# Kernel optimization log

Measured on AMD Instinct MI355X. Metric: run time of the kernel, lower is better.

The kernel has to match this reference:

```python
import jax, jax.numpy as jnp
import numpy as np

UP_RATIO = 2
DOWN_RATIO = 2
K = 12  # hard-coded filter size assumed by the fused kernel


def kaiser_sinc_filter1d(cutoff, half_width, kernel_size):
    # Exact replica of BigVGAN's kaiser_sinc_filter1d (even kernel branch).
    half_size = kernel_size // 2
    delta_f = 4.0 * half_width
    A = 2.285 * (half_size - 1) * np.pi * delta_f + 7.95
    if A > 50.0:
        beta = 0.1102 * (A - 8.7)
    elif A >= 21.0:
        beta = 0.5842 * (A - 21.0) ** 0.4 + 0.07886 * (A - 21.0)
    else:
        beta = 0.0
    window = np.kaiser(kernel_size, beta)  # symmetric, == torch.kaiser_window(periodic=False)
    time = np.arange(-half_size, half_size) + 0.5  # even kernel size
    filt = 2.0 * cutoff * window * np.sinc(2.0 * cutoff * time)
    filt = filt / filt.sum()
    return filt.astype(np.float32)


def setup_inputs() -> dict:
    key = jax.random.key(0)
    k1, k2, k3 = jax.random.split(key, 3)
    B, C, T = 16, 512, 8192
    x = jax.random.normal(k1, (B, C, T), dtype=jnp.float32)
    # log-scale SnakeBeta parameters (alpha_logscale=True -> params stored in log space)
    alpha = jax.random.normal(k2, (C,), dtype=jnp.float32) * 0.1
    beta = jax.random.normal(k3, (C,), dtype=jnp.float32) * 0.1
    up_filter = jnp.asarray(kaiser_sinc_filter1d(0.5 / UP_RATIO, 0.6 / UP_RATIO, K))
    down_filter = jnp.asarray(kaiser_sinc_filter1d(0.5 / DOWN_RATIO, 0.6 / DOWN_RATIO, K))
    return {"x": x, "up_filter": up_filter, "down_filter": down_filter,
            "alpha": alpha, "beta": beta}


def _depthwise_conv(x, filt, stride=1, lhs_dilation=1, pad=(0, 0)):
    # x: (B, C, T); shared 1-tap-bank depthwise conv: fold channels into batch.
    B, C, T = x.shape
    xr = x.reshape(B * C, 1, T)
    w = filt.reshape(1, 1, -1)
    out = jax.lax.conv_general_dilated(
        xr, w, window_strides=(stride,), padding=[pad],
        lhs_dilation=(lhs_dilation,),
        dimension_numbers=("NCH", "OIH", "NCH"))
    return out.reshape(B, C, -1)


def reference(x, up_filter, down_filter, alpha, beta):
    B, C, T = x.shape
    # ---- UpSample1d(ratio=2, kernel_size=12): replicate pad + conv_transpose ----
    pad = K // UP_RATIO - 1                              # 5
    pad_left = pad * UP_RATIO + (K - UP_RATIO) // 2      # 15
    pad_right = pad * UP_RATIO + (K - UP_RATIO + 1) // 2  # 15
    xp = jnp.pad(x, ((0, 0), (0, 0), (pad, pad)), mode="edge")
    # conv_transpose1d(stride=s) == lhs-dilated conv with flipped kernel, full padding
    up = UP_RATIO * _depthwise_conv(xp, up_filter[::-1],
                                    lhs_dilation=UP_RATIO, pad=(K - 1, K - 1))
    up = up[..., pad_left: up.shape[-1] - pad_right]      # (B, C, 2T)
    # ---- SnakeBeta activation (log-scale alpha/beta) ----
    a = jnp.exp(alpha)[None, :, None]
    b = jnp.exp(beta)[None, :, None]
    act = up + (1.0 / (b + 1e-9)) * jnp.sin(up * a) ** 2
    # ---- DownSample1d: replicate-padded lowpass FIR, stride 2 ----
    dl = K // 2 - 1   # 5 (even kernel)
    dr = K // 2       # 6
    actp = jnp.pad(act, ((0, 0), (0, 0), (dl, dr)), mode="edge")
    out = _depthwise_conv(actp, down_filter, stride=DOWN_RATIO)  # (B, C, T)
    return out
```

## Files before the change

### kernel.cpp

```cpp
#include <hip/hip_runtime.h>


#define T_LEN 8192
#define C_CH  512
#define B_N   16
#define W     8
#define BLOCK 256

__global__ __launch_bounds__(BLOCK) void act1d_kernel(
    const float* __restrict__ x,
    const float* __restrict__ uf_g,
    const float* __restrict__ df_g,
    const float* __restrict__ alpha,
    const float* __restrict__ beta,
    float* __restrict__ out)
{
    const int T = T_LEN;
    const int bid = blockIdx.x;
    const int row = bid >> 2;
    const int chunk = bid & 3;
    const int c = row & (C_CH - 1);
    const int nb = chunk * (BLOCK * W) + (int)threadIdx.x * W;
    const long rowoff = (long)row * T;
    const float* xrow = x + rowoff;

    float uf[12], df[12];
#pragma unroll
    for (int k = 0; k < 12; ++k) { uf[k] = 2.0f * uf_g[k]; df[k] = df_g[k]; }

    const float ea   = __expf(alpha[c]);
    const float invb = 1.0f / (__expf(beta[c]) + 1e-9f);

    float a[26];

    const bool interior = (nb >= 8) && (nb + 16 <= T);
    if (interior) {
        float xr[24];
        const float4* xv = (const float4*)(xrow + nb - 8);
#pragma unroll
        for (int k = 0; k < 6; ++k) {
            float4 v = xv[k];
            xr[4*k+0] = v.x; xr[4*k+1] = v.y; xr[4*k+2] = v.z; xr[4*k+3] = v.w;
        }
#pragma unroll
        for (int j = 0; j < 26; ++j) {
            const int xi = ((j - 5) >> 1) + 8;
            float up;
            if ((j & 1) == 0) {
                up = uf[0]*xr[xi+3] + uf[2]*xr[xi+2] + uf[4]*xr[xi+1]
                   + uf[6]*xr[xi]   + uf[8]*xr[xi-1] + uf[10]*xr[xi-2];
            } else {
                up = uf[1]*xr[xi+2] + uf[3]*xr[xi+1] + uf[5]*xr[xi]
                   + uf[7]*xr[xi-1] + uf[9]*xr[xi-2] + uf[11]*xr[xi-3];
            }
            const float sv = __sinf(up * ea);
            a[j] = fmaf(invb * sv, sv, up);
        }
    } else {
#pragma unroll
        for (int j = 0; j < 26; ++j) {
            int t = 2*nb - 5 + j;
            t = min(max(t, 0), 2*T - 1);
            const int s = t >> 1;
            const int par = t & 1;
            float xv7[7];
#pragma unroll
            for (int m = 0; m < 7; ++m) {
                int g = s - 3 + m;
                g = min(max(g, 0), T - 1);
                xv7[m] = xrow[g];
            }
            const float upo = uf[0]*xv7[6] + uf[2]*xv7[5] + uf[4]*xv7[4]
                            + uf[6]*xv7[3] + uf[8]*xv7[2] + uf[10]*xv7[1];
            const float upe = uf[1]*xv7[5] + uf[3]*xv7[4] + uf[5]*xv7[3]
                            + uf[7]*xv7[2] + uf[9]*xv7[1] + uf[11]*xv7[0];
            const float up = par ? upo : upe;
            const float sv = __sinf(up * ea);
            a[j] = fmaf(invb * sv, sv, up);
        }
    }

    float o[W];
#pragma unroll
    for (int d = 0; d < W; ++d) {
        float acc = 0.0f;
#pragma unroll
        for (int k = 0; k < 12; ++k) acc = fmaf(df[k], a[2*d + k], acc);
        o[d] = acc;
    }
    float4* ov = (float4*)(out + rowoff + nb);
    ov[0] = make_float4(o[0], o[1], o[2], o[3]);
    ov[1] = make_float4(o[4], o[5], o[6], o[7]);
}

extern "C" void kernel_launch(void* const* d_in, const int* in_sizes, int n_in,
                              void* d_out, int out_size, void* d_ws, size_t ws_size,
                              hipStream_t stream) {
    const float* x  = (const float*)d_in[0];
    const float* uf = (const float*)d_in[1];
    const float* df = (const float*)d_in[2];
    const float* al = (const float*)d_in[3];
    const float* be = (const float*)d_in[4];
    float* outp = (float*)d_out;

    const int grid = B_N * C_CH * (T_LEN / (BLOCK * W));
    act1d_kernel<<<grid, BLOCK, 0, stream>>>(x, uf, df, al, be, outp);
}
```

Before: 466.0 us.

## Use packed FP32 math, raw hardware sine, and nontemporal stores in fused kernel

```diff
diff --git a/kernel.cpp b/kernel.cpp
--- a/kernel.cpp
+++ b/kernel.cpp
@@ -6,6 +6,31 @@
 #define B_N   16
 #define W     8
 #define BLOCK 256
+
+typedef float f2 __attribute__((ext_vector_type(2)));
+typedef float f4 __attribute__((ext_vector_type(4)));
+
+__device__ __forceinline__ f2 pk_mul(f2 a, f2 b) {
+    f2 d; asm("v_pk_mul_f32 %0, %1, %2" : "=v"(d) : "v"(a), "v"(b)); return d;
+}
+__device__ __forceinline__ f2 pk_mul_bx(f2 a, f2 b) {
+    f2 d; asm("v_pk_mul_f32 %0, %1, %2 op_sel:[0,0] op_sel_hi:[1,0]" : "=v"(d) : "v"(a), "v"(b)); return d;
+}
+__device__ __forceinline__ f2 pk_mul_by(f2 a, f2 b) {
+    f2 d; asm("v_pk_mul_f32 %0, %1, %2 op_sel:[0,1] op_sel_hi:[1,1]" : "=v"(d) : "v"(a), "v"(b)); return d;
+}
+__device__ __forceinline__ void pk_fma(f2& acc, f2 a, f2 b) {
+    asm("v_pk_fma_f32 %0, %1, %2, %0" : "+v"(acc) : "v"(a), "v"(b));
+}
+__device__ __forceinline__ void pk_fma_bx(f2& acc, f2 a, f2 b) {
+    asm("v_pk_fma_f32 %0, %1, %2, %0 op_sel:[0,0,0] op_sel_hi:[1,0,1]" : "+v"(acc) : "v"(a), "v"(b));
+}
+__device__ __forceinline__ void pk_fma_by(f2& acc, f2 a, f2 b) {
+    asm("v_pk_fma_f32 %0, %1, %2, %0 op_sel:[0,1,0] op_sel_hi:[1,1,1]" : "+v"(acc) : "v"(a), "v"(b));
+}
+__device__ __forceinline__ float hw_sin(float x_rev) {
+    float r; asm("v_sin_f32 %0, %1" : "=v"(r) : "v"(x_rev)); return r;
+}
 
 __global__ __launch_bounds__(BLOCK) void act1d_kernel(
     const float* __restrict__ x,
@@ -24,37 +49,53 @@
     const long rowoff = (long)row * T;
     const float* xrow = x + rowoff;
 
-    float uf[12], df[12];
+    f2 ufp[6], dfp[6];
+    const f2* ufv = (const f2*)uf_g;
+    const f2* dfv = (const f2*)df_g;
 #pragma unroll
-    for (int k = 0; k < 12; ++k) { uf[k] = 2.0f * uf_g[k]; df[k] = df_g[k]; }
+    for (int m = 0; m < 6; ++m) {
+        f2 u = ufv[m];
+        ufp[m].x = 2.0f * u.x; ufp[m].y = 2.0f * u.y;
+        dfp[m] = dfv[m];
+    }
 
-    const float ea   = __expf(alpha[c]);
+    const float ea_r = __expf(alpha[c]) * 0.15915494309189535f;
     const float invb = 1.0f / (__expf(beta[c]) + 1e-9f);
+    f2 eap; eap.x = ea_r; eap.y = ea_r;
+    f2 ibp; ibp.x = invb; ibp.y = invb;
 
-    float a[26];
+    f2 a2[13];
 
     const bool interior = (nb >= 8) && (nb + 16 <= T);
     if (interior) {
-        float xr[24];
-        const float4* xv = (const float4*)(xrow + nb - 8);
+        f2 xx[12];
+        const f4* xv4 = (const f4*)(xrow + nb - 8);
 #pragma unroll
         for (int k = 0; k < 6; ++k) {
-            float4 v = xv[k];
-            xr[4*k+0] = v.x; xr[4*k+1] = v.y; xr[4*k+2] = v.z; xr[4*k+3] = v.w;
+            f4 v = xv4[k];
+            xx[2*k].x   = v.x; xx[2*k].y   = v.y;
+            xx[2*k+1].x = v.z; xx[2*k+1].y = v.w;
         }
 #pragma unroll
-        for (int j = 0; j < 26; ++j) {
-            const int xi = ((j - 5) >> 1) + 8;
-            float up;
-            if ((j & 1) == 0) {
-                up = uf[0]*xr[xi+3] + uf[2]*xr[xi+2] + uf[4]*xr[xi+1]
-                   + uf[6]*xr[xi]   + uf[8]*xr[xi-1] + uf[10]*xr[xi-2];
-            } else {
-                up = uf[1]*xr[xi+2] + uf[3]*xr[xi+1] + uf[5]*xr[xi]
-                   + uf[7]*xr[xi-1] + uf[9]*xr[xi-2] + uf[11]*xr[xi-3];
+        for (int p = 0; p < 13; ++p) {
+            f2 u;
+            {
+                const int w = p + 8;
+                if (w & 1) u = pk_mul_by(ufp[0], xx[w >> 1]);
+                else       u = pk_mul_bx(ufp[0], xx[w >> 1]);
             }
-            const float sv = __sinf(up * ea);
-            a[j] = fmaf(invb * sv, sv, up);
+#pragma unroll
+            for (int m = 1; m < 6; ++m) {
+                const int w = p + 8 - m;
+                if (w & 1) pk_fma_by(u, ufp[m], xx[w >> 1]);
+                else       pk_fma_bx(u, ufp[m], xx[w >> 1]);
+            }
+            f2 s = pk_mul(u, eap);
+            f2 sv; sv.x = hw_sin(s.x); sv.y = hw_sin(s.y);
+            f2 t = pk_mul(sv, ibp);
+            f2 av = u;
+            pk_fma(av, t, sv);
+            a2[p] = av;
         }
     } else {
 #pragma unroll
@@ -70,27 +111,30 @@
                 g = min(max(g, 0), T - 1);
                 xv7[m] = xrow[g];
             }
-            const float upo = uf[0]*xv7[6] + uf[2]*xv7[5] + uf[4]*xv7[4]
-                            + uf[6]*xv7[3] + uf[8]*xv7[2] + uf[10]*xv7[1];
-            const float upe = uf[1]*xv7[5] + uf[3]*xv7[4] + uf[5]*xv7[3]
-                            + uf[7]*xv7[2] + uf[9]*xv7[1] + uf[11]*xv7[0];
+            const float upo = ufp[0].x*xv7[6] + ufp[1].x*xv7[5] + ufp[2].x*xv7[4]
+                            + ufp[3].x*xv7[3] + ufp[4].x*xv7[2] + ufp[5].x*xv7[1];
+            const float upe = ufp[0].y*xv7[5] + ufp[1].y*xv7[4] + ufp[2].y*xv7[3]
+                            + ufp[3].y*xv7[2] + ufp[4].y*xv7[1] + ufp[5].y*xv7[0];
             const float up = par ? upo : upe;
-            const float sv = __sinf(up * ea);
-            a[j] = fmaf(invb * sv, sv, up);
+            const float sv = hw_sin(up * ea_r);
+            const float aj = fmaf(invb * sv, sv, up);
+            if (j & 1) a2[j >> 1].y = aj; else a2[j >> 1].x = aj;
         }
     }
 
     float o[W];
 #pragma unroll
     for (int d = 0; d < W; ++d) {
-        float acc = 0.0f;
+        f2 acc = pk_mul(dfp[0], a2[d]);
 #pragma unroll
-        for (int k = 0; k < 12; ++k) acc = fmaf(df[k], a[2*d + k], acc);
-        o[d] = acc;
+        for (int m = 1; m < 6; ++m) pk_fma(acc, dfp[m], a2[d + m]);
+        o[d] = acc.x + acc.y;
     }
-    float4* ov = (float4*)(out + rowoff + nb);
-    ov[0] = make_float4(o[0], o[1], o[2], o[3]);
-    ov[1] = make_float4(o[4], o[5], o[6], o[7]);
+    f4* ov = (f4*)(out + rowoff + nb);
+    f4 o0; o0.x = o[0]; o0.y = o[1]; o0.z = o[2]; o0.w = o[3];
+    f4 o1; o1.x = o[4]; o1.y = o[5]; o1.z = o[6]; o1.w = o[7];
+    __builtin_nontemporal_store(o0, ov);
+    __builtin_nontemporal_store(o1, ov + 1);
 }
 
 extern "C" void kernel_launch(void* const* d_in, const int* in_sizes, int n_in,
```

Result: no change. 463.7 us (-0.5%).
